# Kernel tuning notes

Measured on AMD Instinct MI355X. Metric: run time of the kernel, lower is better.

The kernel has to match this reference:

```python
import jax, jax.numpy as jnp
import numpy as np

B, C, H, W = 8, 256, 48, 48
RED = 1  # reduction
CR = C // RED
CG = C // 4  # fuse gate hidden channels


def conv1x1(x, w):
    # x: [B,C,H,W], w: [O,C] -> [B,O,H,W]
    return jnp.einsum('oc,bchw->bohw', w, x)


def conv3x3(x, w, b):
    # x: [B,Ci,H,W], w: [O,Ci,3,3], b: [O]
    y = jax.lax.conv_general_dilated(
        x, w, window_strides=(1, 1), padding='SAME',
        dimension_numbers=('NCHW', 'OIHW', 'NCHW'))
    return y + b[None, :, None, None]


def cross_attention(source, guidance, wq, wk, wv, bv, gamma):
    b, c, h, w = source.shape
    hw = h * w
    Q = conv1x1(source, wq).reshape(b, -1, hw)      # [B,CR,HW]
    K = conv1x1(guidance, wk).reshape(b, -1, hw)    # [B,CR,HW]
    V = (conv1x1(guidance, wv) + bv[None, :, None, None]).reshape(b, c, hw)
    energy = jnp.einsum('bqn,bqm->bnm', Q, K)       # [B,HW,HW]
    attn = jax.nn.softmax(energy, axis=-1)
    out = jnp.einsum('bcm,bnm->bcn', V, attn)       # [B,C,HW]
    return gamma * out.reshape(b, c, h, w) + source


def setup_inputs() -> dict:
    key = jax.random.key(0)
    ks = jax.random.split(key, 16)
    s = lambda fan_in: 1.0 / np.sqrt(fan_in)
    d = {
        'x1': jax.random.normal(ks[0], (B, C, H, W), jnp.float32),
        'x2': jax.random.normal(ks[1], (B, C, H, W), jnp.float32),
        'wq1': jax.random.normal(ks[2], (CR, C), jnp.float32) * s(C),
        'wk1': jax.random.normal(ks[3], (CR, C), jnp.float32) * s(C),
        'wv1': jax.random.normal(ks[4], (C, C), jnp.float32) * s(C),
        'bv1': jax.random.normal(ks[5], (C,), jnp.float32) * s(C),
        'gamma1': jax.random.normal(ks[6], (1,), jnp.float32) * 0.1,
        'wq2': jax.random.normal(ks[7], (CR, C), jnp.float32) * s(C),
        'wk2': jax.random.normal(ks[8], (CR, C), jnp.float32) * s(C),
        'wv2': jax.random.normal(ks[9], (C, C), jnp.float32) * s(C),
        'bv2': jax.random.normal(ks[10], (C,), jnp.float32) * s(C),
        'gamma2': jax.random.normal(ks[11], (1,), jnp.float32) * 0.1,
        'fw1': jax.random.normal(ks[12], (CG, 2 * C, 3, 3), jnp.float32) * s(2 * C * 9),
        'fb1': jnp.zeros((CG,), jnp.float32),
        'fw2': jax.random.normal(ks[13], (2, CG, 3, 3), jnp.float32) * s(CG * 9),
        'fb2': jnp.zeros((2,), jnp.float32),
    }
    return d


def reference(x1, x2, wq1, wk1, wv1, bv1, gamma1, wq2, wk2, wv2, bv2, gamma2,
              fw1, fb1, fw2, fb2):
    att_x1 = cross_attention(x1, x2, wq1, wk1, wv1, bv1, gamma1)
    att_x2 = cross_attention(x2, x1, wq2, wk2, wv2, bv2, gamma2)
    cat = jnp.concatenate([att_x1, att_x2], axis=1)  # [B,2C,H,W]
    h = jax.nn.relu(conv3x3(cat, fw1, fb1))
    gates = jax.nn.softmax(conv3x3(h, fw2, fb2), axis=1)  # [B,2,H,W]
    return gates[:, 0:1] * att_x1 + gates[:, 1:2] * att_x2
```

## Files before the change

kernel.cpp:

```cpp
#include <hip/hip_runtime.h>

namespace {

constexpr int BATCH = 8;
constexpr int CH    = 256;
constexpr int HW    = 2304;
constexpr int IMG   = 48;
constexpr int CG    = 64;

typedef __bf16 bf16x8 __attribute__((ext_vector_type(8)));
typedef __bf16 bf16x4 __attribute__((ext_vector_type(4)));
typedef float  f32x4  __attribute__((ext_vector_type(4)));

constexpr int ROWB = 40;
constexpr int KSTRD = 136;
constexpr int VSTRD = 68;
constexpr int PSTRD = 132;
constexpr int CSTR = 40;

constexpr size_t BF_SLAB = (size_t)BATCH * HW * CH * 2;
constexpr size_t QT1_OFF = 0;
constexpr size_t KT1_OFF = 1 * BF_SLAB;
constexpr size_t VB1_OFF = 2 * BF_SLAB;
constexpr size_t QT2_OFF = 3 * BF_SLAB;
constexpr size_t KT2_OFF = 4 * BF_SLAB;
constexpr size_t VB2_OFF = 5 * BF_SLAB;
constexpr size_t AT_OFF  = 6 * BF_SLAB;
constexpr size_t A1_OFF  = AT_OFF + (size_t)BATCH * HW * 512 * 2;
constexpr size_t A2_OFF  = A1_OFF + (size_t)BATCH * CH * HW * 4;
constexpr size_t HB_OFF  = A2_OFF + (size_t)BATCH * CH * HW * 4;
constexpr size_t G0_OFF  = HB_OFF + (size_t)BATCH * CG * HW * 4;
constexpr size_t WT_OFF  = G0_OFF + (size_t)BATCH * HW * 4;

__device__ __forceinline__ void stage_bf16(const __bf16* __restrict__ src, size_t srcStride,
                                           __bf16* dst, int t) {
    const int r = t & 127, s = t >> 7;
    const bf16x8* sp = reinterpret_cast<const bf16x8*>(src + (size_t)r * srcStride + s * 16);
    bf16x8* dp = reinterpret_cast<bf16x8*>(dst + r * ROWB + s * 16);
    dp[0] = sp[0];
    dp[1] = sp[1];
}

__device__ __forceinline__ void stage_f32(const float* __restrict__ src, size_t srcStride,
                                          __bf16* dst, int t) {
    const int r = t & 127, s = t >> 7;
    const float4* sp = reinterpret_cast<const float4*>(src + (size_t)r * srcStride + s * 16);
    float4 f0 = sp[0], f1 = sp[1], f2 = sp[2], f3 = sp[3];
    bf16x8 v0, v1;
    v0[0]=(__bf16)f0.x; v0[1]=(__bf16)f0.y; v0[2]=(__bf16)f0.z; v0[3]=(__bf16)f0.w;
    v0[4]=(__bf16)f1.x; v0[5]=(__bf16)f1.y; v0[6]=(__bf16)f1.z; v0[7]=(__bf16)f1.w;
    v1[0]=(__bf16)f2.x; v1[1]=(__bf16)f2.y; v1[2]=(__bf16)f2.z; v1[3]=(__bf16)f2.w;
    v1[4]=(__bf16)f3.x; v1[5]=(__bf16)f3.y; v1[6]=(__bf16)f3.z; v1[7]=(__bf16)f3.w;
    bf16x8* dp = reinterpret_cast<bf16x8*>(dst + r * ROWB + s * 16);
    dp[0] = v0;
    dp[1] = v1;
}

__device__ __forceinline__ void frag_step(const __bf16* As, const __bf16* Bs,
                                          f32x4 (&acc)[4][4], int lane, int wm, int wn) {
    const int r = lane & 15, g = lane >> 4;
    bf16x8 a[4], b[4];
#pragma unroll
    for (int i = 0; i < 4; ++i) {
        a[i] = *reinterpret_cast<const bf16x8*>(As + (wm * 64 + i * 16 + r) * ROWB + g * 8);
        b[i] = *reinterpret_cast<const bf16x8*>(Bs + (wn * 64 + i * 16 + r) * ROWB + g * 8);
    }
#pragma unroll
    for (int i = 0; i < 4; ++i)
#pragma unroll
        for (int j = 0; j < 4; ++j)
            acc[i][j] = __builtin_amdgcn_mfma_f32_16x16x32_bf16(a[i], b[j], acc[i][j], 0, 0, 0);
}

__global__ __launch_bounds__(256) void proj3_mfma(
    const float* __restrict__ Xsrc, const float* __restrict__ Xg,
    const float* __restrict__ wq, const float* __restrict__ wk,
    const float* __restrict__ wv, const float* __restrict__ bv,
    __bf16* __restrict__ QT, __bf16* __restrict__ KT, __bf16* __restrict__ VB)
{
    __shared__ __bf16 As[128 * ROWB];
    __shared__ __bf16 Bs[128 * ROWB];
    const int p = blockIdx.z >> 3;
    const int b = blockIdx.z & 7;
    const float* W = (p == 0) ? wq : (p == 1) ? wk : wv;
    const float* X = (p == 0) ? Xsrc : Xg;
    const float* Xb = X + (size_t)b * CH * HW;

    const int t = threadIdx.x;
    const int lane = t & 63, wid = t >> 6;
    const int wm = wid >> 1, wn = wid & 1;
    const int m0 = blockIdx.y * 128, n0 = blockIdx.x * 128;

    f32x4 acc[4][4] = {};
    const int nB = t & 127, halfB = t >> 7;

    for (int k0 = 0; k0 < CH; k0 += 32) {
        stage_f32(W + (size_t)m0 * CH + k0, CH, As, t);
        float v[16];
#pragma unroll
        for (int kk = 0; kk < 16; ++kk)
            v[kk] = Xb[(size_t)(k0 + halfB * 16 + kk) * HW + n0 + nB];
        bf16x8 p0, p1;
#pragma unroll
        for (int kk = 0; kk < 8; ++kk) { p0[kk] = (__bf16)v[kk]; p1[kk] = (__bf16)v[kk + 8]; }
        bf16x8* dp = reinterpret_cast<bf16x8*>(Bs + nB * ROWB + halfB * 16);
        dp[0] = p0; dp[1] = p1;
        __syncthreads();
        frag_step(As, Bs, acc, lane, wm, wn);
        __syncthreads();
    }

    const int g = lane >> 4, r = lane & 15;
    if (p < 2) {
        __bf16* T = (p == 0) ? QT : KT;
#pragma unroll
        for (int mi = 0; mi < 4; ++mi)
#pragma unroll
            for (int nj = 0; nj < 4; ++nj) {
                const int mb = m0 + wm * 64 + mi * 16 + g * 4;
                const int n  = n0 + wn * 64 + nj * 16 + r;
                bf16x4 pk;
#pragma unroll
                for (int q = 0; q < 4; ++q) pk[q] = (__bf16)acc[mi][nj][q];
                *reinterpret_cast<bf16x4*>(T + ((size_t)b * HW + n) * CH + mb) = pk;
            }
    } else {
#pragma unroll
        for (int mi = 0; mi < 4; ++mi)
#pragma unroll
            for (int nj = 0; nj < 4; ++nj) {
                const int mb = m0 + wm * 64 + mi * 16 + g * 4;
                const int n  = n0 + wn * 64 + nj * 16 + r;
#pragma unroll
                for (int q = 0; q < 4; ++q)
                    VB[((size_t)b * CH + mb + q) * HW + n] = (__bf16)(acc[mi][nj][q] + bv[mb + q]);
            }
    }
}

__global__ __launch_bounds__(256, 3) void fused_flash(
    const __bf16* __restrict__ QT1, const __bf16* __restrict__ KT1, const __bf16* __restrict__ VB1,
    const __bf16* __restrict__ QT2, const __bf16* __restrict__ KT2, const __bf16* __restrict__ VB2,
    const float* __restrict__ x1, const float* __restrict__ x2,
    const float* __restrict__ g1, const float* __restrict__ g2,
    float* __restrict__ A1, float* __restrict__ A2, __bf16* __restrict__ AT)
{
    __shared__ __bf16 KV[17408];
    __shared__ __bf16 P_lds[64 * PSTRD];
    __shared__ float  sc_lds[64];
    __bf16* Ks = KV;
    __bf16* Vs = KV;

    const int bid  = blockIdx.x;
    const int work = (bid & 7) * 72 + (bid >> 3);
    const int z = work / 36, ntile = work - z * 36;

    const int att = z >> 3, b = z & 7;
    const __bf16* QT = att ? QT2 : QT1;
    const __bf16* KT = att ? KT2 : KT1;
    const __bf16* VB = att ? VB2 : VB1;
    const float* src = att ? x2 : x1;
    const float* gmp = att ? g2 : g1;
    float* A         = att ? A2 : A1;
    const int aoff   = att ? CH : 0;

    const int t = threadIdx.x, lane = t & 63, w = t >> 6;
    const int r = lane & 15, g = lane >> 4;
    const int n0 = ntile * 64;

    bf16x8 qf[8];
    {
        const __bf16* qrow = QT + ((size_t)b * HW + n0 + w * 16 + r) * CH;
#pragma unroll
        for (int kc = 0; kc < 8; ++kc)
            qf[kc] = *reinterpret_cast<const bf16x8*>(qrow + kc * 32 + g * 8);
    }

    float m_run = -3.0e38f;
    float s_run = 0.f;
    f32x4 accO[4][4] = {};

    for (int m0 = 0; m0 < HW; m0 += 128) {
        f32x4 accS[8] = {};
#pragma unroll
        for (int kh = 0; kh < 2; ++kh) {
            {
                const int kr = t >> 1, kcol = (t & 1) * 64;
                const bf16x8* sp = reinterpret_cast<const bf16x8*>(
                    KT + ((size_t)b * HW + m0 + kr) * CH + kh * 128 + kcol);
                bf16x8* dp = reinterpret_cast<bf16x8*>(Ks + kr * KSTRD + kcol);
#pragma unroll
                for (int u = 0; u < 8; ++u) dp[u] = sp[u];
            }
            __syncthreads();
            __builtin_amdgcn_s_setprio(1);
#pragma unroll
            for (int kk = 0; kk < 4; ++kk) {
                const bf16x8 qv = qf[kh * 4 + kk];
#pragma unroll
                for (int j = 0; j < 8; ++j) {
                    const bf16x8 kf = *reinterpret_cast<const bf16x8*>(
                        Ks + (j * 16 + r) * KSTRD + kk * 32 + g * 8);
                    accS[j] = __builtin_amdgcn_mfma_f32_16x16x32_bf16(kf, qv, accS[j], 0, 0, 0);
                }
            }
            __builtin_amdgcn_s_setprio(0);
            __syncthreads();
        }
        {
            float tmax = accS[0][0];
#pragma unroll
            for (int j = 0; j < 8; ++j)
#pragma unroll
                for (int q = 0; q < 4; ++q) tmax = fmaxf(tmax, accS[j][q]);
            tmax = fmaxf(tmax, __shfl_xor(tmax, 16));
            tmax = fmaxf(tmax, __shfl_xor(tmax, 32));
            const float nm = fmaxf(m_run, tmax);
            float ts = 0.f;
#pragma unroll
            for (int j = 0; j < 8; ++j) {
                const float pe0 = __expf(accS[j][0] - nm);
                const float pe1 = __expf(accS[j][1] - nm);
                const float pe2 = __expf(accS[j][2] - nm);
                const float pe3 = __expf(accS[j][3] - nm);
                ts += (pe0 + pe1) + (pe2 + pe3);
                bf16x4 pk;
                pk[0] = (__bf16)pe0; pk[1] = (__bf16)pe1;
                pk[2] = (__bf16)pe2; pk[3] = (__bf16)pe3;
                *reinterpret_cast<bf16x4*>(
                    P_lds + (w * 16 + r) * PSTRD + j * 16 + g * 4) = pk;
            }
            ts += __shfl_xor(ts, 16);
            ts += __shfl_xor(ts, 32);
            const float scale = __expf(m_run - nm);
            s_run = s_run * scale + ts;
            m_run = nm;
            if (lane < 16) sc_lds[w * 16 + r] = scale;
        }
        __syncthreads();
        {
            float scj[4];
#pragma unroll
            for (int j = 0; j < 4; ++j) scj[j] = sc_lds[j * 16 + r];
#pragma unroll
            for (int i = 0; i < 4; ++i)
#pragma unroll
                for (int j = 0; j < 4; ++j)
#pragma unroll
                    for (int q = 0; q < 4; ++q) accO[i][j][q] *= scj[j];
        }
#pragma unroll 1
        for (int vc = 0; vc < 2; ++vc) {
            {
                const bf16x8* sv = reinterpret_cast<const bf16x8*>(
                    VB + ((size_t)b * CH + t) * HW + m0 + vc * 64);
                bf16x8* dv = reinterpret_cast<bf16x8*>(Vs + t * VSTRD);
#pragma unroll
                for (int u = 0; u < 8; ++u) dv[u] = sv[u];
            }
            __syncthreads();
            __builtin_amdgcn_s_setprio(1);
#pragma unroll
            for (int kk = 0; kk < 2; ++kk) {
                bf16x8 av[4], bp[4];
#pragma unroll
                for (int i = 0; i < 4; ++i)
                    av[i] = *reinterpret_cast<const bf16x8*>(
                        Vs + (w * 64 + i * 16 + r) * VSTRD + kk * 32 + g * 8);
#pragma unroll
                for (int j = 0; j < 4; ++j)
                    bp[j] = *reinterpret_cast<const bf16x8*>(
                        P_lds + (j * 16 + r) * PSTRD + vc * 64 + kk * 32 + g * 8);
#pragma unroll
                for (int i = 0; i < 4; ++i)
#pragma unroll
                    for (int j = 0; j < 4; ++j)
                        accO[i][j] = __builtin_amdgcn_mfma_f32_16x16x32_bf16(av[i], bp[j], accO[i][j], 0, 0, 0);
            }
            __builtin_amdgcn_s_setprio(0);
            __syncthreads();
        }
    }

    if (lane < 16) sc_lds[w * 16 + r] = 1.f / s_run;
    __syncthreads();
    float IS_l[4];
#pragma unroll
    for (int j = 0; j < 4; ++j) IS_l[j] = sc_lds[j * 16 + r];
    const float gm = gmp[0];
#pragma unroll
    for (int i = 0; i < 4; ++i)
#pragma unroll
        for (int j = 0; j < 4; ++j) {
            const int cb = w * 64 + i * 16 + g * 4;
            const int n  = n0 + j * 16 + r;
            const float sc = gm * IS_l[j];
            float vals[4];
#pragma unroll
            for (int q = 0; q < 4; ++q) {
                const size_t idx = ((size_t)b * CH + cb + q) * HW + n;
                vals[q] = sc * accO[i][j][q] + src[idx];
                A[idx] = vals[q];
            }
            bf16x4 pk;
#pragma unroll
            for (int q = 0; q < 4; ++q) pk[q] = (__bf16)vals[q];
            *reinterpret_cast<bf16x4*>(AT + ((size_t)b * HW + n) * 512 + aoff + cb) = pk;
        }
}

__global__ __launch_bounds__(256) void wprep(const float* __restrict__ fw1,
                                             __bf16* __restrict__ WT)
{
    const int i = blockIdx.x * 256 + threadIdx.x;
    const int tap = i >> 15;
    const int rem = i & 32767;
    const int m = rem >> 9, c = rem & 511;
    WT[i] = (__bf16)fw1[(size_t)m * 4608 + c * 9 + tap];
}

__global__ __launch_bounds__(256) void conv1_v2(
    const __bf16* __restrict__ AT, const __bf16* __restrict__ WT,
    float* __restrict__ P4)
{
    __shared__ __bf16 A9[9 * 64 * CSTR];
    __shared__ __bf16 HALO[240 * CSTR];
    const int kc = blockIdx.y, b = blockIdx.z, n0 = blockIdx.x * 128;
    const int t = threadIdx.x, lane = t & 63, wid = t >> 6;
    const int r = lane & 15, g = lane >> 4;

    int yj[2], xj[2];
#pragma unroll
    for (int j = 0; j < 2; ++j) {
        const int p = n0 + wid * 32 + j * 16 + r;
        yj[j] = p / IMG; xj[j] = p - yj[j] * IMG;
    }

    f32x4 acc[4][2] = {};

#pragma unroll 1
    for (int st = 0; st < 4; ++st) {
        const int cbase = kc * 128 + st * 32;
        if (t < 240) {
            const int nn = n0 - 56 + t;
            bf16x8 h0 = {}, h1 = {}, h2 = {}, h3 = {};
            if (nn >= 0 && nn < HW) {
                const bf16x8* sp = reinterpret_cast<const bf16x8*>(
                    AT + ((size_t)b * HW + nn) * 512 + cbase);
                h0 = sp[0]; h1 = sp[1]; h2 = sp[2]; h3 = sp[3];
            }
            bf16x8* dp = reinterpret_cast<bf16x8*>(HALO + t * CSTR);
            dp[0] = h0; dp[1] = h1; dp[2] = h2; dp[3] = h3;
        }
        {
            const int m = t >> 2, seg = t & 3;
#pragma unroll
            for (int tap = 0; tap < 9; ++tap)
                *reinterpret_cast<bf16x8*>(A9 + (tap * 64 + m) * CSTR + seg * 8) =
                    *reinterpret_cast<const bf16x8*>(WT + ((size_t)tap * 64 + m) * 512 + cbase + seg * 8);
        }
        __syncthreads();
#pragma unroll 1
        for (int tap = 0; tap < 9; ++tap) {
            const int dy = tap / 3 - 1;
            const int dx = tap - (tap / 3) * 3 - 1;
            bf16x8 bb[2];
#pragma unroll
            for (int j = 0; j < 2; ++j) {
                const bool valid = ((unsigned)(yj[j] + dy) < (unsigned)IMG) &&
                                   ((unsigned)(xj[j] + dx) < (unsigned)IMG);
                const int row = wid * 32 + j * 16 + r + 56 + dy * IMG + dx;
                bf16x8 v = {};
                if (valid) v = *reinterpret_cast<const bf16x8*>(HALO + row * CSTR + g * 8);
                bb[j] = v;
            }
            bf16x8 a[4];
#pragma unroll
            for (int i = 0; i < 4; ++i)
                a[i] = *reinterpret_cast<const bf16x8*>(A9 + (tap * 64 + i * 16 + r) * CSTR + g * 8);
#pragma unroll
            for (int i = 0; i < 4; ++i)
#pragma unroll
                for (int j = 0; j < 2; ++j)
                    acc[i][j] = __builtin_amdgcn_mfma_f32_16x16x32_bf16(a[i], bb[j], acc[i][j], 0, 0, 0);
        }
        __syncthreads();
    }
#pragma unroll
    for (int mi = 0; mi < 4; ++mi)
#pragma unroll
        for (int nj = 0; nj < 2; ++nj) {
            const int m = mi * 16 + g * 4;
            const int n = n0 + wid * 32 + nj * 16 + r;
#pragma unroll
            for (int q = 0; q < 4; ++q)
                P4[(((size_t)kc * BATCH + b) * CG + m + q) * HW + n] = acc[mi][nj][q];
        }
}

__global__ __launch_bounds__(256) void reduce_hb(
    const float* __restrict__ P4, const float* __restrict__ fb1,
    float* __restrict__ HB)
{
    const int idx = blockIdx.x * 256 + threadIdx.x;
    constexpr size_t STRIDE = (size_t)BATCH * CG * HW;
    const int m = (idx / HW) & 63;
    float s = P4[idx] + P4[idx + STRIDE] + P4[idx + 2 * STRIDE] + P4[idx + 3 * STRIDE];
    HB[idx] = fmaxf(s + fb1[m], 0.f);
}

__global__ __launch_bounds__(256) void gates_v2(
    const float* __restrict__ hbuf, const float* __restrict__ fw2,
    const float* __restrict__ fb2, float* __restrict__ g0buf)
{
    __shared__ float w2s[1152];
    __shared__ float par[2][4][64];
    const int t = threadIdx.x;
    for (int i = t; i < 1152; i += 256) w2s[i] = fw2[i];
    __syncthreads();
    const int px = t & 63, grp = t >> 6;
    const int idx = blockIdx.x * 64 + px;
    const int b = idx / HW;
    const int n = idx - b * HW;
    const int y = n / IMG, x = n - (n / IMG) * IMG;
    float c0 = 0.f, c1 = 0.f;
    const float* hb = hbuf + ((size_t)b * CG + grp * 16) * HW;
    for (int ci = 0; ci < 16; ++ci) {
        const float* hp = hb + (size_t)ci * HW;
        const float* w0 = &w2s[(grp * 16 + ci) * 9];
        const float* w1 = &w2s[576 + (grp * 16 + ci) * 9];
#pragma unroll
        for (int tap = 0; tap < 9; ++tap) {
            const int dy = tap / 3 - 1, dx = tap % 3 - 1;
            const int yy = y + dy, xx = x + dx;
            if (yy >= 0 && yy < IMG && xx >= 0 && xx < IMG) {
                const float hv = hp[yy * IMG + xx];
                c0 = fmaf(hv, w0[tap], c0);
                c1 = fmaf(hv, w1[tap], c1);
            }
        }
    }
    par[0][grp][px] = c0;
    par[1][grp][px] = c1;
    __syncthreads();
    if (t < 64) {
        const float s0 = par[0][0][t] + par[0][1][t] + par[0][2][t] + par[0][3][t] + fb2[0];
        const float s1 = par[1][0][t] + par[1][1][t] + par[1][2][t] + par[1][3][t] + fb2[1];
        g0buf[blockIdx.x * 64 + t] = 1.f / (1.f + __expf(s1 - s0));
    }
}

__global__ __launch_bounds__(256) void blend_kernel(
    const float* __restrict__ att1, const float* __restrict__ att2,
    const float* __restrict__ g0buf, float* __restrict__ out)
{
    const int i = blockIdx.x * 256 + threadIdx.x;
    const int r = i / 576;
    const int q = i - r * 576;
    const int b = r >> 8;
    const float4 a1 = reinterpret_cast<const float4*>(att1)[i];
    const float4 a2 = reinterpret_cast<const float4*>(att2)[i];
    const float4 g  = *reinterpret_cast<const float4*>(&g0buf[(size_t)b * HW + q * 4]);
    float4 o;
    o.x = g.x * a1.x + (1.f - g.x) * a2.x;
    o.y = g.y * a1.y + (1.f - g.y) * a2.y;
    o.z = g.z * a1.z + (1.f - g.z) * a2.z;
    o.w = g.w * a1.w + (1.f - g.w) * a2.w;
    reinterpret_cast<float4*>(out)[i] = o;
}

}

extern "C" void kernel_launch(void* const* d_in, const int* in_sizes, int n_in,
                              void* d_out, int out_size, void* d_ws, size_t ws_size,
                              hipStream_t stream)
{
    const float* x1  = (const float*)d_in[0];
    const float* x2  = (const float*)d_in[1];
    const float* wq1 = (const float*)d_in[2];
    const float* wk1 = (const float*)d_in[3];
    const float* wv1 = (const float*)d_in[4];
    const float* bv1 = (const float*)d_in[5];
    const float* g1  = (const float*)d_in[6];
    const float* wq2 = (const float*)d_in[7];
    const float* wk2 = (const float*)d_in[8];
    const float* wv2 = (const float*)d_in[9];
    const float* bv2 = (const float*)d_in[10];
    const float* g2  = (const float*)d_in[11];
    const float* fw1 = (const float*)d_in[12];
    const float* fb1 = (const float*)d_in[13];
    const float* fw2 = (const float*)d_in[14];
    const float* fb2 = (const float*)d_in[15];
    float* out = (float*)d_out;
    char*  wsb = (char*)d_ws;

    __bf16* QT1 = (__bf16*)(wsb + QT1_OFF);
    __bf16* KT1 = (__bf16*)(wsb + KT1_OFF);
    __bf16* VB1 = (__bf16*)(wsb + VB1_OFF);
    __bf16* QT2 = (__bf16*)(wsb + QT2_OFF);
    __bf16* KT2 = (__bf16*)(wsb + KT2_OFF);
    __bf16* VB2 = (__bf16*)(wsb + VB2_OFF);
    __bf16* AT  = (__bf16*)(wsb + AT_OFF);
    float*  A1  = (float*)(wsb + A1_OFF);
    float*  A2  = (float*)(wsb + A2_OFF);
    float*  HB  = (float*)(wsb + HB_OFF);
    float*  G0  = (float*)(wsb + G0_OFF);
    __bf16* WT  = (__bf16*)(wsb + WT_OFF);
    float*  P4  = (float*)(wsb + QT1_OFF);

    (void)in_sizes; (void)n_in; (void)out_size; (void)ws_size;

    proj3_mfma<<<dim3(18, 2, 24), 256, 0, stream>>>(x1, x2, wq1, wk1, wv1, bv1, QT1, KT1, VB1);
    proj3_mfma<<<dim3(18, 2, 24), 256, 0, stream>>>(x2, x1, wq2, wk2, wv2, bv2, QT2, KT2, VB2);
    wprep<<<dim3(1152), 256, 0, stream>>>(fw1, WT);

    fused_flash<<<dim3(576), 256, 0, stream>>>(
        QT1, KT1, VB1, QT2, KT2, VB2, x1, x2, g1, g2, A1, A2, AT);

    conv1_v2<<<dim3(18, 4, 8), 256, 0, stream>>>(AT, WT, P4);
    reduce_hb<<<dim3(4608), 256, 0, stream>>>(P4, fb1, HB);
    gates_v2<<<dim3(288), 256, 0, stream>>>(HB, fw2, fb2, G0);
    blend_kernel<<<dim3(4608), 256, 0, stream>>>(A1, A2, G0, out);
}
```

Baseline: 478.6 us.

## Prefetch K tiles into registers and load V fragments directly from global

Restructures the flash-attention loop so the next K half-tile is prefetched into registers while MFMAs run on the current LDS tile. V fragments are read straight from global memory into registers (av0/av1) instead of being staged through LDS, which removes the V staging barriers. The max and sum reductions use trees instead of serial chains, and launch bounds drop from 3 to 2 waves to make room for the extra registers. This may lower occupancy, and the direct V reads from global are strided.

```diff
diff --git a/kernel.cpp b/kernel.cpp
--- a/kernel.cpp
+++ b/kernel.cpp
@@ -14,8 +14,7 @@
 
 constexpr int ROWB = 40;
 constexpr int KSTRD = 136;
-constexpr int VSTRD = 68;
-constexpr int PSTRD = 132;
+constexpr int PSTRD = 136;
 constexpr int CSTR = 40;
 
 constexpr size_t BF_SLAB = (size_t)BATCH * HW * CH * 2;
@@ -32,15 +31,6 @@
 constexpr size_t G0_OFF  = HB_OFF + (size_t)BATCH * CG * HW * 4;
 constexpr size_t WT_OFF  = G0_OFF + (size_t)BATCH * HW * 4;
 
-__device__ __forceinline__ void stage_bf16(const __bf16* __restrict__ src, size_t srcStride,
-                                           __bf16* dst, int t) {
-    const int r = t & 127, s = t >> 7;
-    const bf16x8* sp = reinterpret_cast<const bf16x8*>(src + (size_t)r * srcStride + s * 16);
-    bf16x8* dp = reinterpret_cast<bf16x8*>(dst + r * ROWB + s * 16);
-    dp[0] = sp[0];
-    dp[1] = sp[1];
-}
-
 __device__ __forceinline__ void stage_f32(const float* __restrict__ src, size_t srcStride,
                                           __bf16* dst, int t) {
     const int r = t & 127, s = t >> 7;
@@ -138,18 +128,16 @@
     }
 }
 
-__global__ __launch_bounds__(256, 3) void fused_flash(
+__global__ __launch_bounds__(256, 2) void fused_flash(
     const __bf16* __restrict__ QT1, const __bf16* __restrict__ KT1, const __bf16* __restrict__ VB1,
     const __bf16* __restrict__ QT2, const __bf16* __restrict__ KT2, const __bf16* __restrict__ VB2,
     const float* __restrict__ x1, const float* __restrict__ x2,
     const float* __restrict__ g1, const float* __restrict__ g2,
     float* __restrict__ A1, float* __restrict__ A2, __bf16* __restrict__ AT)
 {
-    __shared__ __bf16 KV[17408];
+    __shared__ __bf16 Ks[128 * KSTRD];
     __shared__ __bf16 P_lds[64 * PSTRD];
     __shared__ float  sc_lds[64];
-    __bf16* Ks = KV;
-    __bf16* Vs = KV;
 
     const int bid  = blockIdx.x;
     const int work = (bid & 7) * 72 + (bid >> 3);
@@ -167,6 +155,8 @@
     const int t = threadIdx.x, lane = t & 63, w = t >> 6;
     const int r = lane & 15, g = lane >> 4;
     const int n0 = ntile * 64;
+    const __bf16* KTb = KT + (size_t)b * HW * CH;
+    const __bf16* VBb = VB + (size_t)b * CH * HW;
 
     bf16x8 qf[8];
     {
@@ -176,60 +166,104 @@
             qf[kc] = *reinterpret_cast<const bf16x8*>(qrow + kc * 32 + g * 8);
     }
 
+    const int kr = t >> 1, kcol = (t & 1) * 64;
+    bf16x8 kbuf[8];
+    {
+        const bf16x8* sp = reinterpret_cast<const bf16x8*>(KTb + (size_t)kr * CH + kcol);
+#pragma unroll
+        for (int u = 0; u < 8; ++u) kbuf[u] = sp[u];
+    }
+
     float m_run = -3.0e38f;
     float s_run = 0.f;
     f32x4 accO[4][4] = {};
 
     for (int m0 = 0; m0 < HW; m0 += 128) {
         f32x4 accS[8] = {};
-#pragma unroll
-        for (int kh = 0; kh < 2; ++kh) {
-            {
-                const int kr = t >> 1, kcol = (t & 1) * 64;
-                const bf16x8* sp = reinterpret_cast<const bf16x8*>(
-                    KT + ((size_t)b * HW + m0 + kr) * CH + kh * 128 + kcol);
-                bf16x8* dp = reinterpret_cast<bf16x8*>(Ks + kr * KSTRD + kcol);
-#pragma unroll
-                for (int u = 0; u < 8; ++u) dp[u] = sp[u];
-            }
-            __syncthreads();
-            __builtin_amdgcn_s_setprio(1);
-#pragma unroll
-            for (int kk = 0; kk < 4; ++kk) {
-                const bf16x8 qv = qf[kh * 4 + kk];
-#pragma unroll
-                for (int j = 0; j < 8; ++j) {
-                    const bf16x8 kf = *reinterpret_cast<const bf16x8*>(
-                        Ks + (j * 16 + r) * KSTRD + kk * 32 + g * 8);
-                    accS[j] = __builtin_amdgcn_mfma_f32_16x16x32_bf16(kf, qv, accS[j], 0, 0, 0);
-                }
-            }
-            __builtin_amdgcn_s_setprio(0);
-            __syncthreads();
-        }
-        {
-            float tmax = accS[0][0];
+        {
+            bf16x8* dp = reinterpret_cast<bf16x8*>(Ks + kr * KSTRD + kcol);
+#pragma unroll
+            for (int u = 0; u < 8; ++u) dp[u] = kbuf[u];
+        }
+        __syncthreads();
+        {
+            const bf16x8* sp = reinterpret_cast<const bf16x8*>(
+                KTb + (size_t)(m0 + kr) * CH + 128 + kcol);
+#pragma unroll
+            for (int u = 0; u < 8; ++u) kbuf[u] = sp[u];
+        }
+        __builtin_amdgcn_s_setprio(1);
+#pragma unroll
+        for (int kk = 0; kk < 4; ++kk) {
+            const bf16x8 qv = qf[kk];
+#pragma unroll
+            for (int j = 0; j < 8; ++j) {
+                const bf16x8 kf = *reinterpret_cast<const bf16x8*>(
+                    Ks + (j * 16 + r) * KSTRD + kk * 32 + g * 8);
+                accS[j] = __builtin_amdgcn_mfma_f32_16x16x32_bf16(kf, qv, accS[j], 0, 0, 0);
+            }
+        }
+        __builtin_amdgcn_s_setprio(0);
+        __syncthreads();
+        {
+            bf16x8* dp = reinterpret_cast<bf16x8*>(Ks + kr * KSTRD + kcol);
+#pragma unroll
+            for (int u = 0; u < 8; ++u) dp[u] = kbuf[u];
+        }
+        __syncthreads();
+        {
+            const int m0n = (m0 + 128 < HW) ? (m0 + 128) : 0;
+            const bf16x8* sp = reinterpret_cast<const bf16x8*>(
+                KTb + (size_t)(m0n + kr) * CH + kcol);
+#pragma unroll
+            for (int u = 0; u < 8; ++u) kbuf[u] = sp[u];
+        }
+        bf16x8 av0[8];
+#pragma unroll
+        for (int kk = 0; kk < 2; ++kk)
+#pragma unroll
+            for (int i = 0; i < 4; ++i)
+                av0[kk * 4 + i] = *reinterpret_cast<const bf16x8*>(
+                    VBb + (size_t)(w * 64 + i * 16 + r) * HW + m0 + kk * 32 + g * 8);
+        __builtin_amdgcn_s_setprio(1);
+#pragma unroll
+        for (int kk = 0; kk < 4; ++kk) {
+            const bf16x8 qv = qf[4 + kk];
+#pragma unroll
+            for (int j = 0; j < 8; ++j) {
+                const bf16x8 kf = *reinterpret_cast<const bf16x8*>(
+                    Ks + (j * 16 + r) * KSTRD + kk * 32 + g * 8);
+                accS[j] = __builtin_amdgcn_mfma_f32_16x16x32_bf16(kf, qv, accS[j], 0, 0, 0);
+            }
+        }
+        __builtin_amdgcn_s_setprio(0);
+        {
+            float mj[8];
 #pragma unroll
             for (int j = 0; j < 8; ++j)
-#pragma unroll
-                for (int q = 0; q < 4; ++q) tmax = fmaxf(tmax, accS[j][q]);
+                mj[j] = fmaxf(fmaxf(accS[j][0], accS[j][1]), fmaxf(accS[j][2], accS[j][3]));
+            float m03 = fmaxf(fmaxf(mj[0], mj[1]), fmaxf(mj[2], mj[3]));
+            float m47 = fmaxf(fmaxf(mj[4], mj[5]), fmaxf(mj[6], mj[7]));
+            float tmax = fmaxf(m03, m47);
             tmax = fmaxf(tmax, __shfl_xor(tmax, 16));
             tmax = fmaxf(tmax, __shfl_xor(tmax, 32));
             const float nm = fmaxf(m_run, tmax);
-            float ts = 0.f;
+            float tsj[8];
 #pragma unroll
             for (int j = 0; j < 8; ++j) {
                 const float pe0 = __expf(accS[j][0] - nm);
                 const float pe1 = __expf(accS[j][1] - nm);
                 const float pe2 = __expf(accS[j][2] - nm);
                 const float pe3 = __expf(accS[j][3] - nm);
-                ts += (pe0 + pe1) + (pe2 + pe3);
+                tsj[j] = (pe0 + pe1) + (pe2 + pe3);
                 bf16x4 pk;
                 pk[0] = (__bf16)pe0; pk[1] = (__bf16)pe1;
                 pk[2] = (__bf16)pe2; pk[3] = (__bf16)pe3;
                 *reinterpret_cast<bf16x4*>(
                     P_lds + (w * 16 + r) * PSTRD + j * 16 + g * 4) = pk;
             }
+            float ts = ((tsj[0] + tsj[1]) + (tsj[2] + tsj[3])) +
+                       ((tsj[4] + tsj[5]) + (tsj[6] + tsj[7]));
             ts += __shfl_xor(ts, 16);
             ts += __shfl_xor(ts, 32);
             const float scale = __expf(m_run - nm);
@@ -249,37 +283,43 @@
 #pragma unroll
                     for (int q = 0; q < 4; ++q) accO[i][j][q] *= scj[j];
         }
-#pragma unroll 1
-        for (int vc = 0; vc < 2; ++vc) {
-            {
-                const bf16x8* sv = reinterpret_cast<const bf16x8*>(
-                    VB + ((size_t)b * CH + t) * HW + m0 + vc * 64);
-                bf16x8* dv = reinterpret_cast<bf16x8*>(Vs + t * VSTRD);
-#pragma unroll
-                for (int u = 0; u < 8; ++u) dv[u] = sv[u];
-            }
-            __syncthreads();
-            __builtin_amdgcn_s_setprio(1);
-#pragma unroll
-            for (int kk = 0; kk < 2; ++kk) {
-                bf16x8 av[4], bp[4];
-#pragma unroll
-                for (int i = 0; i < 4; ++i)
-                    av[i] = *reinterpret_cast<const bf16x8*>(
-                        Vs + (w * 64 + i * 16 + r) * VSTRD + kk * 32 + g * 8);
+        bf16x8 av1[8];
+#pragma unroll
+        for (int kk = 0; kk < 2; ++kk)
+#pragma unroll
+            for (int i = 0; i < 4; ++i)
+                av1[kk * 4 + i] = *reinterpret_cast<const bf16x8*>(
+                    VBb + (size_t)(w * 64 + i * 16 + r) * HW + m0 + 64 + kk * 32 + g * 8);
+        __builtin_amdgcn_s_setprio(1);
+#pragma unroll
+        for (int kk = 0; kk < 2; ++kk) {
+            bf16x8 bp[4];
+#pragma unroll
+            for (int j = 0; j < 4; ++j)
+                bp[j] = *reinterpret_cast<const bf16x8*>(
+                    P_lds + (j * 16 + r) * PSTRD + kk * 32 + g * 8);
+#pragma unroll
+            for (int i = 0; i < 4; ++i)
 #pragma unroll
                 for (int j = 0; j < 4; ++j)
-                    bp[j] = *reinterpret_cast<const bf16x8*>(
-                        P_lds + (j * 16 + r) * PSTRD + vc * 64 + kk * 32 + g * 8);
-#pragma unroll
-                for (int i = 0; i < 4; ++i)
-#pragma unroll
-                    for (int j = 0; j < 4; ++j)
-                        accO[i][j] = __builtin_amdgcn_mfma_f32_16x16x32_bf16(av[i], bp[j], accO[i][j], 0, 0, 0);
-            }
-            __builtin_amdgcn_s_setprio(0);
-            __syncthreads();
-        }
+                    accO[i][j] = __builtin_amdgcn_mfma_f32_16x16x32_bf16(
+                        av0[kk * 4 + i], bp[j], accO[i][j], 0, 0, 0);
+        }
+#pragma unroll
+        for (int kk = 0; kk < 2; ++kk) {
+            bf16x8 bp[4];
+#pragma unroll
+            for (int j = 0; j < 4; ++j)
+                bp[j] = *reinterpret_cast<const bf16x8*>(
+                    P_lds + (j * 16 + r) * PSTRD + 64 + kk * 32 + g * 8);
+#pragma unroll
+            for (int i = 0; i < 4; ++i)
+#pragma unroll
+                for (int j = 0; j < 4; ++j)
+                    accO[i][j] = __builtin_amdgcn_mfma_f32_16x16x32_bf16(
+                        av1[kk * 4 + i], bp[j], accO[i][j], 0, 0, 0);
+        }
+        __builtin_amdgcn_s_setprio(0);
     }
 
     if (lane < 16) sc_lds[w * 16 + r] = 1.f / s_run;
```

Result: faster. 396.3 us (-17.2%).

## Pipeline K tiles via async global-to-LDS DMA ring and read V directly

Applied to the files above, without the earlier changes.

Replaces the synchronous K staging in the flash-attention kernel with a triple-buffered ring filled by global_load_lds DMA. Loads for quarter-chunks two steps ahead are issued early and waited on with explicit vmcnt barriers, and the LDS layout uses an XOR swizzle to avoid bank conflicts. V is no longer staged through LDS; each wave reads its V fragments straight from global memory. This removes several block barriers per tile and overlaps K loads with MFMA work. The costs are more LDS per block, lowered occupancy (launch bounds 3 to 2), and uncoalesced-ish direct global V reads.

```diff
diff --git a/kernel.cpp b/kernel.cpp
--- a/kernel.cpp
+++ b/kernel.cpp
@@ -13,10 +13,9 @@
 typedef float  f32x4  __attribute__((ext_vector_type(4)));
 
 constexpr int ROWB = 40;
-constexpr int KSTRD = 136;
-constexpr int VSTRD = 68;
-constexpr int PSTRD = 132;
+constexpr int PSTRD = 136;
 constexpr int CSTR = 40;
+constexpr int KQ_ELE = 8192;
 
 constexpr size_t BF_SLAB = (size_t)BATCH * HW * CH * 2;
 constexpr size_t QT1_OFF = 0;
@@ -32,13 +31,25 @@
 constexpr size_t G0_OFF  = HB_OFF + (size_t)BATCH * CG * HW * 4;
 constexpr size_t WT_OFF  = G0_OFF + (size_t)BATCH * HW * 4;
 
-__device__ __forceinline__ void stage_bf16(const __bf16* __restrict__ src, size_t srcStride,
-                                           __bf16* dst, int t) {
-    const int r = t & 127, s = t >> 7;
-    const bf16x8* sp = reinterpret_cast<const bf16x8*>(src + (size_t)r * srcStride + s * 16);
-    bf16x8* dp = reinterpret_cast<bf16x8*>(dst + r * ROWB + s * 16);
-    dp[0] = sp[0];
-    dp[1] = sp[1];
+__device__ __forceinline__ void dma16(const __bf16* g, __bf16* l) {
+    __builtin_amdgcn_global_load_lds(
+        (const __attribute__((address_space(1))) void*)g,
+        (__attribute__((address_space(3))) void*)l,
+        16, 0, 0);
+}
+
+__device__ __forceinline__ void issue_k_dma(const __bf16* __restrict__ KTb,
+                                            __bf16* Kslot, int m0_i, int qq,
+                                            int w, int lane) {
+    const int lrow = lane >> 3;
+    const int lg   = (lane & 7) ^ lrow;
+    const int colb = qq * 64 + lg * 8;
+#pragma unroll
+    for (int qi = 0; qi < 4; ++qi) {
+        const int row = (w * 4 + qi) * 8 + lrow;
+        dma16(KTb + (size_t)(m0_i + row) * CH + colb,
+              Kslot + (w * 4 + qi) * 512);
+    }
 }
 
 __device__ __forceinline__ void stage_f32(const float* __restrict__ src, size_t srcStride,
@@ -138,18 +149,16 @@
     }
 }
 
-__global__ __launch_bounds__(256, 3) void fused_flash(
+__global__ __launch_bounds__(256, 2) void fused_flash(
     const __bf16* __restrict__ QT1, const __bf16* __restrict__ KT1, const __bf16* __restrict__ VB1,
     const __bf16* __restrict__ QT2, const __bf16* __restrict__ KT2, const __bf16* __restrict__ VB2,
     const float* __restrict__ x1, const float* __restrict__ x2,
     const float* __restrict__ g1, const float* __restrict__ g2,
     float* __restrict__ A1, float* __restrict__ A2, __bf16* __restrict__ AT)
 {
-    __shared__ __bf16 KV[17408];
+    __shared__ __bf16 Ks[3 * KQ_ELE];
     __shared__ __bf16 P_lds[64 * PSTRD];
     __shared__ float  sc_lds[64];
-    __bf16* Ks = KV;
-    __bf16* Vs = KV;
 
     const int bid  = blockIdx.x;
     const int work = (bid & 7) * 72 + (bid >> 3);
@@ -166,7 +175,10 @@
 
     const int t = threadIdx.x, lane = t & 63, w = t >> 6;
     const int r = lane & 15, g = lane >> 4;
+    const int rs7 = r & 7;
     const int n0 = ntile * 64;
+    const __bf16* KTb = KT + (size_t)b * HW * CH;
+    const __bf16* VBb = VB + (size_t)b * CH * HW;
 
     bf16x8 qf[8];
     {
@@ -176,60 +188,73 @@
             qf[kc] = *reinterpret_cast<const bf16x8*>(qrow + kc * 32 + g * 8);
     }
 
+    issue_k_dma(KTb, Ks, 0, 0, w, lane);
+    issue_k_dma(KTb, Ks + KQ_ELE, 0, 1, w, lane);
+
     float m_run = -3.0e38f;
     float s_run = 0.f;
     f32x4 accO[4][4] = {};
-
-    for (int m0 = 0; m0 < HW; m0 += 128) {
+    int base_t = 0;
+
+    for (int tile = 0; tile < 18; ++tile) {
+        const int m0 = tile * 128;
         f32x4 accS[8] = {};
 #pragma unroll
-        for (int kh = 0; kh < 2; ++kh) {
+        for (int q = 0; q < 4; ++q) {
+            asm volatile("s_waitcnt vmcnt(4)\n\ts_barrier" ::: "memory");
             {
-                const int kr = t >> 1, kcol = (t & 1) * 64;
-                const bf16x8* sp = reinterpret_cast<const bf16x8*>(
-                    KT + ((size_t)b * HW + m0 + kr) * CH + kh * 128 + kcol);
-                bf16x8* dp = reinterpret_cast<bf16x8*>(Ks + kr * KSTRD + kcol);
-#pragma unroll
-                for (int u = 0; u < 8; ++u) dp[u] = sp[u];
-            }
-            __syncthreads();
+                int qq_i = q + 2;
+                int m0_i = m0;
+                if (qq_i >= 4) { qq_i -= 4; m0_i = (tile == 17) ? 0 : m0 + 128; }
+                int slot_i = base_t + q + 2;
+                if (slot_i >= 3) slot_i -= 3;
+                if (slot_i >= 3) slot_i -= 3;
+                issue_k_dma(KTb, Ks + slot_i * KQ_ELE, m0_i, qq_i, w, lane);
+            }
+            int slot = base_t + q;
+            if (slot >= 3) slot -= 3;
+            const __bf16* Kq = Ks + slot * KQ_ELE;
             __builtin_amdgcn_s_setprio(1);
 #pragma unroll
-            for (int kk = 0; kk < 4; ++kk) {
-                const bf16x8 qv = qf[kh * 4 + kk];
+            for (int kk = 0; kk < 2; ++kk) {
+                const bf16x8 qv = qf[q * 2 + kk];
+                const int swz = ((kk * 4 + g) ^ rs7) * 8;
 #pragma unroll
                 for (int j = 0; j < 8; ++j) {
                     const bf16x8 kf = *reinterpret_cast<const bf16x8*>(
-                        Ks + (j * 16 + r) * KSTRD + kk * 32 + g * 8);
+                        Kq + (j * 16 + r) * 64 + swz);
                     accS[j] = __builtin_amdgcn_mfma_f32_16x16x32_bf16(kf, qv, accS[j], 0, 0, 0);
                 }
             }
             __builtin_amdgcn_s_setprio(0);
-            __syncthreads();
         }
         {
-            float tmax = accS[0][0];
+            float mj[8];
 #pragma unroll
             for (int j = 0; j < 8; ++j)
-#pragma unroll
-                for (int q = 0; q < 4; ++q) tmax = fmaxf(tmax, accS[j][q]);
+                mj[j] = fmaxf(fmaxf(accS[j][0], accS[j][1]), fmaxf(accS[j][2], accS[j][3]));
+            float m03 = fmaxf(fmaxf(mj[0], mj[1]), fmaxf(mj[2], mj[3]));
+            float m47 = fmaxf(fmaxf(mj[4], mj[5]), fmaxf(mj[6], mj[7]));
+            float tmax = fmaxf(m03, m47);
             tmax = fmaxf(tmax, __shfl_xor(tmax, 16));
             tmax = fmaxf(tmax, __shfl_xor(tmax, 32));
             const float nm = fmaxf(m_run, tmax);
-            float ts = 0.f;
+            float tsj[8];
 #pragma unroll
             for (int j = 0; j < 8; ++j) {
                 const float pe0 = __expf(accS[j][0] - nm);
                 const float pe1 = __expf(accS[j][1] - nm);
                 const float pe2 = __expf(accS[j][2] - nm);
                 const float pe3 = __expf(accS[j][3] - nm);
-                ts += (pe0 + pe1) + (pe2 + pe3);
+                tsj[j] = (pe0 + pe1) + (pe2 + pe3);
                 bf16x4 pk;
                 pk[0] = (__bf16)pe0; pk[1] = (__bf16)pe1;
                 pk[2] = (__bf16)pe2; pk[3] = (__bf16)pe3;
                 *reinterpret_cast<bf16x4*>(
                     P_lds + (w * 16 + r) * PSTRD + j * 16 + g * 4) = pk;
             }
+            float ts = ((tsj[0] + tsj[1]) + (tsj[2] + tsj[3])) +
+                       ((tsj[4] + tsj[5]) + (tsj[6] + tsj[7]));
             ts += __shfl_xor(ts, 16);
             ts += __shfl_xor(ts, 32);
             const float scale = __expf(m_run - nm);
@@ -237,7 +262,7 @@
             m_run = nm;
             if (lane < 16) sc_lds[w * 16 + r] = scale;
         }
-        __syncthreads();
+        asm volatile("s_waitcnt lgkmcnt(0)\n\ts_barrier" ::: "memory");
         {
             float scj[4];
 #pragma unroll
@@ -249,37 +274,31 @@
 #pragma unroll
                     for (int q = 0; q < 4; ++q) accO[i][j][q] *= scj[j];
         }
-#pragma unroll 1
-        for (int vc = 0; vc < 2; ++vc) {
-            {
-                const bf16x8* sv = reinterpret_cast<const bf16x8*>(
-                    VB + ((size_t)b * CH + t) * HW + m0 + vc * 64);
-                bf16x8* dv = reinterpret_cast<bf16x8*>(Vs + t * VSTRD);
-#pragma unroll
-                for (int u = 0; u < 8; ++u) dv[u] = sv[u];
-            }
-            __syncthreads();
-            __builtin_amdgcn_s_setprio(1);
+        __builtin_amdgcn_s_setprio(1);
+#pragma unroll
+        for (int half = 0; half < 2; ++half) {
 #pragma unroll
             for (int kk = 0; kk < 2; ++kk) {
                 bf16x8 av[4], bp[4];
 #pragma unroll
                 for (int i = 0; i < 4; ++i)
                     av[i] = *reinterpret_cast<const bf16x8*>(
-                        Vs + (w * 64 + i * 16 + r) * VSTRD + kk * 32 + g * 8);
+                        VBb + (size_t)(w * 64 + i * 16 + r) * HW + m0 + half * 64 + kk * 32 + g * 8);
 #pragma unroll
                 for (int j = 0; j < 4; ++j)
                     bp[j] = *reinterpret_cast<const bf16x8*>(
-                        P_lds + (j * 16 + r) * PSTRD + vc * 64 + kk * 32 + g * 8);
+                        P_lds + (j * 16 + r) * PSTRD + half * 64 + kk * 32 + g * 8);
 #pragma unroll
                 for (int i = 0; i < 4; ++i)
 #pragma unroll
                     for (int j = 0; j < 4; ++j)
-                        accO[i][j] = __builtin_amdgcn_mfma_f32_16x16x32_bf16(av[i], bp[j], accO[i][j], 0, 0, 0);
-            }
-            __builtin_amdgcn_s_setprio(0);
-            __syncthreads();
-        }
+                        accO[i][j] = __builtin_amdgcn_mfma_f32_16x16x32_bf16(
+                            av[i], bp[j], accO[i][j], 0, 0, 0);
+            }
+        }
+        __builtin_amdgcn_s_setprio(0);
+        base_t += 1;
+        if (base_t == 3) base_t = 0;
     }
 
     if (lane < 16) sc_lds[w * 16 + r] = 1.f / s_run;
```

After: 404.1 us. 15.6% less time.
